# Performance work log

Hardware: AMD Instinct MI355X
Metric: run time of the kernel (lower is better)

The kernel has to match this reference:

```python
import jax, jax.numpy as jnp
import numpy as np

DIM = 192
WIN = 8
HEADS = 6
HEAD_DIM = DIM // HEADS
SCALE = HEAD_DIM ** -0.5
N = WIN * WIN


def _relative_position_index():
    coords = np.stack(np.meshgrid(np.arange(WIN), np.arange(WIN), indexing='ij'))  # [2,W,W]
    flat = coords.reshape(2, -1)  # [2,N]
    rel = flat[:, :, None] - flat[:, None, :]  # [2,N,N]
    rel = rel.transpose(1, 2, 0)
    rel[:, :, 0] += WIN - 1
    rel[:, :, 1] += WIN - 1
    rel[:, :, 0] *= 2 * WIN - 1
    return rel.sum(-1).astype(np.int32)  # [N,N]


def setup_inputs() -> dict:
    key = jax.random.key(0)
    ks = jax.random.split(key, 6)
    B = 4096
    x = jax.random.normal(ks[0], (B, N, DIM), dtype=jnp.float32)
    qkv_w = jax.random.normal(ks[1], (3 * DIM, DIM), dtype=jnp.float32) * (DIM ** -0.5)
    qkv_b = jnp.zeros((3 * DIM,), dtype=jnp.float32)
    proj_w = jax.random.normal(ks[2], (DIM, DIM), dtype=jnp.float32) * (DIM ** -0.5)
    proj_b = jnp.zeros((DIM,), dtype=jnp.float32)
    num_rel = (2 * WIN - 1) * (2 * WIN - 1)
    bias_table = jax.random.normal(ks[3], (num_rel, HEADS), dtype=jnp.float32) * 0.02
    rel_idx = jnp.asarray(_relative_position_index())
    return {"x": x, "qkv_w": qkv_w, "qkv_b": qkv_b, "proj_w": proj_w,
            "proj_b": proj_b, "bias_table": bias_table, "rel_idx": rel_idx}


def reference(x, qkv_w, qkv_b, proj_w, proj_b, bias_table, rel_idx):
    B, n, C = x.shape
    qkv = x @ qkv_w.T + qkv_b  # [B,N,3C]
    qkv = qkv.reshape(B, n, 3, HEADS, HEAD_DIM).transpose(2, 0, 3, 1, 4)  # [3,B,H,N,hd]
    q, k, v = qkv[0], qkv[1], qkv[2]
    attn = jnp.einsum('bhnd,bhmd->bhnm', q * SCALE, k)  # [B,H,N,N]
    bias = bias_table[rel_idx]  # [N,N,H]
    attn = attn + bias.transpose(2, 0, 1)[None]  # add [1,H,N,N]
    attn = jax.nn.softmax(attn, axis=-1)
    out = jnp.einsum('bhnm,bhmd->bhnd', attn, v)
    out = out.transpose(0, 2, 1, 3).reshape(B, n, C)
    return out @ proj_w.T + proj_b
```

## Files before the change

### kernel.cpp

```cpp
#include <hip/hip_runtime.h>

#define NTOK 64
#define DIM 192
#define HEADS 6
#define HD 32
#define SCALE 0.17677669529663687f

typedef __bf16 bf16x8 __attribute__((ext_vector_type(8)));
typedef float f32x4 __attribute__((ext_vector_type(4)));

__device__ __forceinline__ unsigned short f2bf(float f) {
  union { float f; unsigned u; } v; v.f = f;
  unsigned u = v.u;
  return (unsigned short)((u + 0x7FFFu + ((u >> 16) & 1u)) >> 16);
}

__global__ void prep_kernel(const float* __restrict__ qkv_w,
                            const float* __restrict__ proj_w,
                            const float* __restrict__ bias_table,
                            const int* __restrict__ rel_idx,
                            unsigned short* __restrict__ wq,
                            unsigned short* __restrict__ wp,
                            float* __restrict__ biasf) {
  int i = blockIdx.x * 256 + threadIdx.x;
  if (i < 3 * DIM * DIM) wq[i] = f2bf(qkv_w[i]);
  if (i < DIM * DIM) wp[i] = f2bf(proj_w[i]);
  if (i < HEADS * NTOK * NTOK) {
    int h = i >> 12;
    int nm = i & 4095;
    biasf[i] = bias_table[rel_idx[nm] * HEADS + h];
  }
}

__global__ __launch_bounds__(384) void attn_kernel(
    const float* __restrict__ x,
    const float* __restrict__ qkv_b,
    const float* __restrict__ proj_b,
    const unsigned short* __restrict__ wq,
    const unsigned short* __restrict__ wp,
    const float* __restrict__ biasf,
    float* __restrict__ out) {
  __shared__ unsigned short xs[NTOK * 200];
  __shared__ unsigned short qs[HEADS * NTOK * HD];
  __shared__ unsigned short kk[HEADS * NTOK * HD];
  __shared__ unsigned short vts[HEADS * HD * 72];
  __shared__ unsigned short Ps[HEADS * NTOK * 72];

  const int tid = threadIdx.x;
  const int w = tid >> 6;
  const int lane = tid & 63;
  const int l15 = lane & 15;
  const int quad = lane >> 4;
  const long b = blockIdx.x;

  {
    const float4* xg = (const float4*)(x + b * (NTOK * DIM));
    #pragma unroll
    for (int it = 0; it < 8; ++it) {
      int idx = tid + it * 384;
      float4 v = xg[idx];
      int row = idx / 48;
      int col = (idx % 48) * 4;
      ushort4 o;
      o.x = f2bf(v.x); o.y = f2bf(v.y); o.z = f2bf(v.z); o.w = f2bf(v.w);
      *(ushort4*)&xs[row * 200 + col] = o;
    }
  }
  __syncthreads();

  for (int i = 0; i < 6; ++i) {
    int jt = w * 6 + i;
    int j = jt * 16 + l15;
    f32x4 acc[4] = {f32x4{0.f,0.f,0.f,0.f}, f32x4{0.f,0.f,0.f,0.f},
                    f32x4{0.f,0.f,0.f,0.f}, f32x4{0.f,0.f,0.f,0.f}};
    #pragma unroll
    for (int ks = 0; ks < 6; ++ks) {
      bf16x8 bw = *(const bf16x8*)(wq + (size_t)j * DIM + ks * 32 + quad * 8);
      #pragma unroll
      for (int rt = 0; rt < 4; ++rt) {
        bf16x8 a = *(const bf16x8*)&xs[(rt * 16 + l15) * 200 + ks * 32 + quad * 8];
        acc[rt] = __builtin_amdgcn_mfma_f32_16x16x32_bf16(a, bw, acc[rt], 0, 0, 0);
      }
    }
    float bj = qkv_b[j];
    int which = jt / 12;
    int ft = jt % 12;
    int h = ft >> 1;
    int d = (ft & 1) * 16 + l15;
    if (which == 0) {
      #pragma unroll
      for (int rt = 0; rt < 4; ++rt)
        #pragma unroll
        for (int g = 0; g < 4; ++g) {
          int row = rt * 16 + quad * 4 + g;
          qs[(h * NTOK + row) * HD + d] = f2bf((acc[rt][g] + bj) * SCALE);
        }
    } else if (which == 1) {
      #pragma unroll
      for (int rt = 0; rt < 4; ++rt)
        #pragma unroll
        for (int g = 0; g < 4; ++g) {
          int row = rt * 16 + quad * 4 + g;
          kk[(h * NTOK + row) * HD + d] = f2bf(acc[rt][g] + bj);
        }
    } else {
      #pragma unroll
      for (int rt = 0; rt < 4; ++rt) {
        ushort4 o;
        o.x = f2bf(acc[rt][0] + bj);
        o.y = f2bf(acc[rt][1] + bj);
        o.z = f2bf(acc[rt][2] + bj);
        o.w = f2bf(acc[rt][3] + bj);
        int row0 = rt * 16 + quad * 4;
        *(ushort4*)&vts[(h * HD + d) * 72 + row0] = o;
      }
    }
  }
  __syncthreads();

  {
    const int h = w;
    bf16x8 qa[4], kb[4];
    #pragma unroll
    for (int rt = 0; rt < 4; ++rt)
      qa[rt] = *(const bf16x8*)&qs[(h * NTOK + rt * 16 + l15) * HD + quad * 8];
    #pragma unroll
    for (int ct = 0; ct < 4; ++ct)
      kb[ct] = *(const bf16x8*)&kk[(h * NTOK + ct * 16 + l15) * HD + quad * 8];
    f32x4 s[4][4];
    #pragma unroll
    for (int rt = 0; rt < 4; ++rt)
      #pragma unroll
      for (int ct = 0; ct < 4; ++ct) {
        s[rt][ct] = f32x4{0.f, 0.f, 0.f, 0.f};
        s[rt][ct] = __builtin_amdgcn_mfma_f32_16x16x32_bf16(qa[rt], kb[ct], s[rt][ct], 0, 0, 0);
      }
    const float* bh = biasf + h * 4096;
    #pragma unroll
    for (int rt = 0; rt < 4; ++rt) {
      #pragma unroll
      for (int g = 0; g < 4; ++g) {
        int row = rt * 16 + quad * 4 + g;
        const float* bp = bh + row * 64 + l15;
        float v0 = s[rt][0][g] + bp[0];
        float v1 = s[rt][1][g] + bp[16];
        float v2 = s[rt][2][g] + bp[32];
        float v3 = s[rt][3][g] + bp[48];
        float mx = fmaxf(fmaxf(v0, v1), fmaxf(v2, v3));
        mx = fmaxf(mx, __shfl_xor(mx, 1));
        mx = fmaxf(mx, __shfl_xor(mx, 2));
        mx = fmaxf(mx, __shfl_xor(mx, 4));
        mx = fmaxf(mx, __shfl_xor(mx, 8));
        float e0 = __expf(v0 - mx);
        float e1 = __expf(v1 - mx);
        float e2 = __expf(v2 - mx);
        float e3 = __expf(v3 - mx);
        float sm = e0 + e1 + e2 + e3;
        sm += __shfl_xor(sm, 1);
        sm += __shfl_xor(sm, 2);
        sm += __shfl_xor(sm, 4);
        sm += __shfl_xor(sm, 8);
        float r = __builtin_amdgcn_rcpf(sm);
        int base = (h * NTOK + row) * 72 + l15;
        Ps[base + 0]  = f2bf(e0 * r);
        Ps[base + 16] = f2bf(e1 * r);
        Ps[base + 32] = f2bf(e2 * r);
        Ps[base + 48] = f2bf(e3 * r);
      }
    }
    bf16x8 vb[2][2];
    #pragma unroll
    for (int c2 = 0; c2 < 2; ++c2)
      #pragma unroll
      for (int kv = 0; kv < 2; ++kv)
        vb[c2][kv] = *(const bf16x8*)&vts[(h * HD + c2 * 16 + l15) * 72 + kv * 32 + quad * 8];
    f32x4 o[4][2];
    #pragma unroll
    for (int rt = 0; rt < 4; ++rt)
      #pragma unroll
      for (int c2 = 0; c2 < 2; ++c2)
        o[rt][c2] = f32x4{0.f, 0.f, 0.f, 0.f};
    #pragma unroll
    for (int rt = 0; rt < 4; ++rt)
      #pragma unroll
      for (int kv = 0; kv < 2; ++kv) {
        bf16x8 pa = *(const bf16x8*)&Ps[(h * NTOK + rt * 16 + l15) * 72 + kv * 32 + quad * 8];
        #pragma unroll
        for (int c2 = 0; c2 < 2; ++c2)
          o[rt][c2] = __builtin_amdgcn_mfma_f32_16x16x32_bf16(pa, vb[c2][kv], o[rt][c2], 0, 0, 0);
      }
    #pragma unroll
    for (int rt = 0; rt < 4; ++rt)
      #pragma unroll
      for (int c2 = 0; c2 < 2; ++c2)
        #pragma unroll
        for (int g = 0; g < 4; ++g) {
          int row = rt * 16 + quad * 4 + g;
          xs[row * 200 + h * HD + c2 * 16 + l15] = f2bf(o[rt][c2][g]);
        }
  }
  __syncthreads();

  for (int i = 0; i < 2; ++i) {
    int et = w * 2 + i;
    int e = et * 16 + l15;
    f32x4 acc[4] = {f32x4{0.f,0.f,0.f,0.f}, f32x4{0.f,0.f,0.f,0.f},
                    f32x4{0.f,0.f,0.f,0.f}, f32x4{0.f,0.f,0.f,0.f}};
    #pragma unroll
    for (int ks = 0; ks < 6; ++ks) {
      bf16x8 bw = *(const bf16x8*)(wp + (size_t)e * DIM + ks * 32 + quad * 8);
      #pragma unroll
      for (int rt = 0; rt < 4; ++rt) {
        bf16x8 a = *(const bf16x8*)&xs[(rt * 16 + l15) * 200 + ks * 32 + quad * 8];
        acc[rt] = __builtin_amdgcn_mfma_f32_16x16x32_bf16(a, bw, acc[rt], 0, 0, 0);
      }
    }
    float pb = proj_b[e];
    float* og = out + b * (NTOK * DIM);
    #pragma unroll
    for (int rt = 0; rt < 4; ++rt)
      #pragma unroll
      for (int g = 0; g < 4; ++g) {
        int row = rt * 16 + quad * 4 + g;
        og[row * DIM + e] = acc[rt][g] + pb;
      }
  }
}

extern "C" void kernel_launch(void* const* d_in, const int* in_sizes, int n_in,
                              void* d_out, int out_size, void* d_ws, size_t ws_size,
                              hipStream_t stream) {
  const float* x          = (const float*)d_in[0];
  const float* qkv_w      = (const float*)d_in[1];
  const float* qkv_b      = (const float*)d_in[2];
  const float* proj_w     = (const float*)d_in[3];
  const float* proj_b     = (const float*)d_in[4];
  const float* bias_table = (const float*)d_in[5];
  const int*   rel_idx    = (const int*)d_in[6];

  unsigned short* wq = (unsigned short*)d_ws;
  unsigned short* wp = wq + 3 * DIM * DIM;
  float* biasf = (float*)(wp + DIM * DIM);

  prep_kernel<<<432, 256, 0, stream>>>(qkv_w, proj_w, bias_table, rel_idx, wq, wp, biasf);
  attn_kernel<<<4096, 384, 0, stream>>>(x, qkv_b, proj_b, wq, wp, biasf, (float*)d_out);
}
```

Before: 556.9 us.

## Keep per-head Q/K/V and softmax probabilities in registers, dropping LDS staging

Each wave now computes its own head's Q, K and V projections directly into MFMA operand fragments. A permuted row mapping and transposed products (S^T = K·Q^T) line the outputs up as inputs for the next MFMA, so the qs/kk/vts/Ps shared-memory buffers and their intermediate barrier are gone. This cuts LDS footprint (allowing more blocks per CU) and removes LDS round-trips, and the softmax reduction becomes mostly in-lane. The cost is more register pressure, per-wave weight reloads from global/L2 for the head's 96 rows, and an extra barrier before reusing xs for the attention output.

```diff
diff --git a/kernel.cpp b/kernel.cpp
--- a/kernel.cpp
+++ b/kernel.cpp
@@ -5,9 +5,13 @@
 #define HEADS 6
 #define HD 32
 #define SCALE 0.17677669529663687f
+#define XSS 200
 
 typedef __bf16 bf16x8 __attribute__((ext_vector_type(8)));
 typedef float f32x4 __attribute__((ext_vector_type(4)));
+
+union U8 { bf16x8 v; unsigned short s[8]; };
+union F4 { float4 v; float f[4]; };
 
 __device__ __forceinline__ unsigned short f2bf(float f) {
   union { float f; unsigned u; } v; v.f = f;
@@ -40,11 +44,7 @@
     const unsigned short* __restrict__ wp,
     const float* __restrict__ biasf,
     float* __restrict__ out) {
-  __shared__ unsigned short xs[NTOK * 200];
-  __shared__ unsigned short qs[HEADS * NTOK * HD];
-  __shared__ unsigned short kk[HEADS * NTOK * HD];
-  __shared__ unsigned short vts[HEADS * HD * 72];
-  __shared__ unsigned short Ps[HEADS * NTOK * 72];
+  __shared__ unsigned short xs[NTOK * XSS];
 
   const int tid = threadIdx.x;
   const int w = tid >> 6;
@@ -52,6 +52,7 @@
   const int l15 = lane & 15;
   const int quad = lane >> 4;
   const long b = blockIdx.x;
+  const int h = w;
 
   {
     const float4* xg = (const float4*)(x + b * (NTOK * DIM));
@@ -63,167 +64,173 @@
       int col = (idx % 48) * 4;
       ushort4 o;
       o.x = f2bf(v.x); o.y = f2bf(v.y); o.z = f2bf(v.z); o.w = f2bf(v.w);
-      *(ushort4*)&xs[row * 200 + col] = o;
+      *(ushort4*)&xs[row * XSS + col] = o;
     }
   }
   __syncthreads();
 
-  for (int i = 0; i < 6; ++i) {
-    int jt = w * 6 + i;
-    int j = jt * 16 + l15;
-    f32x4 acc[4] = {f32x4{0.f,0.f,0.f,0.f}, f32x4{0.f,0.f,0.f,0.f},
-                    f32x4{0.f,0.f,0.f,0.f}, f32x4{0.f,0.f,0.f,0.f}};
-    #pragma unroll
-    for (int ks = 0; ks < 6; ++ks) {
-      bf16x8 bw = *(const bf16x8*)(wq + (size_t)j * DIM + ks * 32 + quad * 8);
-      #pragma unroll
-      for (int rt = 0; rt < 4; ++rt) {
-        bf16x8 a = *(const bf16x8*)&xs[(rt * 16 + l15) * 200 + ks * 32 + quad * 8];
-        acc[rt] = __builtin_amdgcn_mfma_f32_16x16x32_bf16(a, bw, acc[rt], 0, 0, 0);
-      }
-    }
-    float bj = qkv_b[j];
-    int which = jt / 12;
-    int ft = jt % 12;
-    int h = ft >> 1;
-    int d = (ft & 1) * 16 + l15;
-    if (which == 0) {
-      #pragma unroll
-      for (int rt = 0; rt < 4; ++rt)
+  const int prm = ((l15 >> 2) << 3) | (l15 & 3);
+  const f32x4 zero = {0.f, 0.f, 0.f, 0.f};
+
+  bf16x8 qfrag[4];
+  {
+    const unsigned short* wqh = wq + ((size_t)h * 32) * DIM;
+    F4 qb0, qb1;
+    qb0.v = *(const float4*)(qkv_b + h * 32 + quad * 8);
+    qb1.v = *(const float4*)(qkv_b + h * 32 + quad * 8 + 4);
+    #pragma unroll
+    for (int nt = 0; nt < 4; ++nt) {
+      bf16x8 xn[6];
+      #pragma unroll
+      for (int ks = 0; ks < 6; ++ks)
+        xn[ks] = *(const bf16x8*)&xs[(nt * 16 + l15) * XSS + ks * 32 + quad * 8];
+      f32x4 a0 = zero, a1 = zero;
+      #pragma unroll
+      for (int ks = 0; ks < 6; ++ks) {
+        bf16x8 w0 = *(const bf16x8*)(wqh + (size_t)(prm + 0) * DIM + ks * 32 + quad * 8);
+        bf16x8 w1 = *(const bf16x8*)(wqh + (size_t)(prm + 4) * DIM + ks * 32 + quad * 8);
+        a0 = __builtin_amdgcn_mfma_f32_16x16x32_bf16(w0, xn[ks], a0, 0, 0, 0);
+        a1 = __builtin_amdgcn_mfma_f32_16x16x32_bf16(w1, xn[ks], a1, 0, 0, 0);
+      }
+      U8 t;
+      #pragma unroll
+      for (int g = 0; g < 4; ++g) {
+        t.s[g]     = f2bf((a0[g] + qb0.f[g]) * SCALE);
+        t.s[4 + g] = f2bf((a1[g] + qb1.f[g]) * SCALE);
+      }
+      qfrag[nt] = t.v;
+    }
+  }
+
+  bf16x8 kfrag[4];
+  U8 vbu[2][2];
+  {
+    const unsigned short* wkh = wq + ((size_t)(192 + h * 32)) * DIM;
+    const unsigned short* wvh = wq + ((size_t)(384 + h * 32)) * DIM;
+    F4 kb0, kb1;
+    kb0.v = *(const float4*)(qkv_b + 192 + h * 32 + quad * 8);
+    kb1.v = *(const float4*)(qkv_b + 192 + h * 32 + quad * 8 + 4);
+    const float vbias0 = qkv_b[384 + h * 32 + l15];
+    const float vbias1 = qkv_b[384 + h * 32 + 16 + l15];
+    #pragma unroll
+    for (int mt = 0; mt < 4; ++mt) {
+      const int kv = mt >> 1, half = mt & 1;
+      const int xrow = kv * 32 + half * 4 + prm;
+      bf16x8 xp[6];
+      #pragma unroll
+      for (int ks = 0; ks < 6; ++ks)
+        xp[ks] = *(const bf16x8*)&xs[xrow * XSS + ks * 32 + quad * 8];
+      f32x4 ka0 = zero, ka1 = zero, va0 = zero, va1 = zero;
+      #pragma unroll
+      for (int ks = 0; ks < 6; ++ks) {
+        bf16x8 wk0 = *(const bf16x8*)(wkh + (size_t)(prm + 0) * DIM + ks * 32 + quad * 8);
+        bf16x8 wk1 = *(const bf16x8*)(wkh + (size_t)(prm + 4) * DIM + ks * 32 + quad * 8);
+        bf16x8 wv0 = *(const bf16x8*)(wvh + (size_t)(l15 + 0) * DIM + ks * 32 + quad * 8);
+        bf16x8 wv1 = *(const bf16x8*)(wvh + (size_t)(l15 + 16) * DIM + ks * 32 + quad * 8);
+        ka0 = __builtin_amdgcn_mfma_f32_16x16x32_bf16(wk0, xp[ks], ka0, 0, 0, 0);
+        ka1 = __builtin_amdgcn_mfma_f32_16x16x32_bf16(wk1, xp[ks], ka1, 0, 0, 0);
+        va0 = __builtin_amdgcn_mfma_f32_16x16x32_bf16(xp[ks], wv0, va0, 0, 0, 0);
+        va1 = __builtin_amdgcn_mfma_f32_16x16x32_bf16(xp[ks], wv1, va1, 0, 0, 0);
+      }
+      U8 t;
+      #pragma unroll
+      for (int g = 0; g < 4; ++g) {
+        t.s[g]     = f2bf(ka0[g] + kb0.f[g]);
+        t.s[4 + g] = f2bf(ka1[g] + kb1.f[g]);
+        vbu[0][kv].s[half * 4 + g] = f2bf(va0[g] + vbias0);
+        vbu[1][kv].s[half * 4 + g] = f2bf(va1[g] + vbias1);
+      }
+      kfrag[mt] = t.v;
+    }
+  }
+
+  f32x4 s[4][4];
+  #pragma unroll
+  for (int mt = 0; mt < 4; ++mt)
+    #pragma unroll
+    for (int nt = 0; nt < 4; ++nt)
+      s[mt][nt] = __builtin_amdgcn_mfma_f32_16x16x32_bf16(kfrag[mt], qfrag[nt], zero, 0, 0, 0);
+
+  bf16x8 pa[4][2];
+  {
+    const float* bh = biasf + h * 4096;
+    #pragma unroll
+    for (int nt = 0; nt < 4; ++nt) {
+      float ve[16];
+      #pragma unroll
+      for (int mt = 0; mt < 4; ++mt) {
+        F4 bb;
+        bb.v = *(const float4*)(bh + (nt * 16 + l15) * 64 + (mt >> 1) * 32 + quad * 8 + (mt & 1) * 4);
         #pragma unroll
-        for (int g = 0; g < 4; ++g) {
-          int row = rt * 16 + quad * 4 + g;
-          qs[(h * NTOK + row) * HD + d] = f2bf((acc[rt][g] + bj) * SCALE);
-        }
-    } else if (which == 1) {
-      #pragma unroll
-      for (int rt = 0; rt < 4; ++rt)
+        for (int g = 0; g < 4; ++g) ve[mt * 4 + g] = s[mt][nt][g] + bb.f[g];
+      }
+      float mx = ve[0];
+      #pragma unroll
+      for (int t = 1; t < 16; ++t) mx = fmaxf(mx, ve[t]);
+      mx = fmaxf(mx, __shfl_xor(mx, 16));
+      mx = fmaxf(mx, __shfl_xor(mx, 32));
+      float sm = 0.f;
+      #pragma unroll
+      for (int t = 0; t < 16; ++t) { ve[t] = __expf(ve[t] - mx); sm += ve[t]; }
+      sm += __shfl_xor(sm, 16);
+      sm += __shfl_xor(sm, 32);
+      float r = __builtin_amdgcn_rcpf(sm);
+      U8 t0, t1;
+      #pragma unroll
+      for (int j = 0; j < 8; ++j) {
+        t0.s[j] = f2bf(ve[j] * r);
+        t1.s[j] = f2bf(ve[8 + j] * r);
+      }
+      pa[nt][0] = t0.v;
+      pa[nt][1] = t1.v;
+    }
+  }
+
+  f32x4 o[4][2];
+  #pragma unroll
+  for (int nt = 0; nt < 4; ++nt)
+    #pragma unroll
+    for (int c2 = 0; c2 < 2; ++c2) {
+      f32x4 acc = __builtin_amdgcn_mfma_f32_16x16x32_bf16(pa[nt][0], vbu[c2][0].v, zero, 0, 0, 0);
+      o[nt][c2] = __builtin_amdgcn_mfma_f32_16x16x32_bf16(pa[nt][1], vbu[c2][1].v, acc, 0, 0, 0);
+    }
+
+  __syncthreads();
+  #pragma unroll
+  for (int nt = 0; nt < 4; ++nt)
+    #pragma unroll
+    for (int c2 = 0; c2 < 2; ++c2)
+      #pragma unroll
+      for (int g = 0; g < 4; ++g)
+        xs[(nt * 16 + quad * 4 + g) * XSS + h * 32 + c2 * 16 + l15] = f2bf(o[nt][c2][g]);
+  __syncthreads();
+
+  {
+    bf16x8 af[4][6];
+    #pragma unroll
+    for (int nt = 0; nt < 4; ++nt)
+      #pragma unroll
+      for (int ks = 0; ks < 6; ++ks)
+        af[nt][ks] = *(const bf16x8*)&xs[(nt * 16 + l15) * XSS + ks * 32 + quad * 8];
+    float* og = out + b * (NTOK * DIM);
+    #pragma unroll
+    for (int i = 0; i < 2; ++i) {
+      const int e = w * 32 + i * 16 + l15;
+      f32x4 acc[4] = {zero, zero, zero, zero};
+      #pragma unroll
+      for (int ks = 0; ks < 6; ++ks) {
+        bf16x8 bw = *(const bf16x8*)(wp + (size_t)e * DIM + ks * 32 + quad * 8);
         #pragma unroll
-        for (int g = 0; g < 4; ++g) {
-          int row = rt * 16 + quad * 4 + g;
-          kk[(h * NTOK + row) * HD + d] = f2bf(acc[rt][g] + bj);
-        }
-    } else {
-      #pragma unroll
-      for (int rt = 0; rt < 4; ++rt) {
-        ushort4 o;
-        o.x = f2bf(acc[rt][0] + bj);
-        o.y = f2bf(acc[rt][1] + bj);
-        o.z = f2bf(acc[rt][2] + bj);
-        o.w = f2bf(acc[rt][3] + bj);
-        int row0 = rt * 16 + quad * 4;
-        *(ushort4*)&vts[(h * HD + d) * 72 + row0] = o;
-      }
-    }
-  }
-  __syncthreads();
-
-  {
-    const int h = w;
-    bf16x8 qa[4], kb[4];
-    #pragma unroll
-    for (int rt = 0; rt < 4; ++rt)
-      qa[rt] = *(const bf16x8*)&qs[(h * NTOK + rt * 16 + l15) * HD + quad * 8];
-    #pragma unroll
-    for (int ct = 0; ct < 4; ++ct)
-      kb[ct] = *(const bf16x8*)&kk[(h * NTOK + ct * 16 + l15) * HD + quad * 8];
-    f32x4 s[4][4];
-    #pragma unroll
-    for (int rt = 0; rt < 4; ++rt)
-      #pragma unroll
-      for (int ct = 0; ct < 4; ++ct) {
-        s[rt][ct] = f32x4{0.f, 0.f, 0.f, 0.f};
-        s[rt][ct] = __builtin_amdgcn_mfma_f32_16x16x32_bf16(qa[rt], kb[ct], s[rt][ct], 0, 0, 0);
-      }
-    const float* bh = biasf + h * 4096;
-    #pragma unroll
-    for (int rt = 0; rt < 4; ++rt) {
-      #pragma unroll
-      for (int g = 0; g < 4; ++g) {
-        int row = rt * 16 + quad * 4 + g;
-        const float* bp = bh + row * 64 + l15;
-        float v0 = s[rt][0][g] + bp[0];
-        float v1 = s[rt][1][g] + bp[16];
-        float v2 = s[rt][2][g] + bp[32];
-        float v3 = s[rt][3][g] + bp[48];
-        float mx = fmaxf(fmaxf(v0, v1), fmaxf(v2, v3));
-        mx = fmaxf(mx, __shfl_xor(mx, 1));
-        mx = fmaxf(mx, __shfl_xor(mx, 2));
-        mx = fmaxf(mx, __shfl_xor(mx, 4));
-        mx = fmaxf(mx, __shfl_xor(mx, 8));
-        float e0 = __expf(v0 - mx);
-        float e1 = __expf(v1 - mx);
-        float e2 = __expf(v2 - mx);
-        float e3 = __expf(v3 - mx);
-        float sm = e0 + e1 + e2 + e3;
-        sm += __shfl_xor(sm, 1);
-        sm += __shfl_xor(sm, 2);
-        sm += __shfl_xor(sm, 4);
-        sm += __shfl_xor(sm, 8);
-        float r = __builtin_amdgcn_rcpf(sm);
-        int base = (h * NTOK + row) * 72 + l15;
-        Ps[base + 0]  = f2bf(e0 * r);
-        Ps[base + 16] = f2bf(e1 * r);
-        Ps[base + 32] = f2bf(e2 * r);
-        Ps[base + 48] = f2bf(e3 * r);
-      }
-    }
-    bf16x8 vb[2][2];
-    #pragma unroll
-    for (int c2 = 0; c2 < 2; ++c2)
-      #pragma unroll
-      for (int kv = 0; kv < 2; ++kv)
-        vb[c2][kv] = *(const bf16x8*)&vts[(h * HD + c2 * 16 + l15) * 72 + kv * 32 + quad * 8];
-    f32x4 o[4][2];
-    #pragma unroll
-    for (int rt = 0; rt < 4; ++rt)
-      #pragma unroll
-      for (int c2 = 0; c2 < 2; ++c2)
-        o[rt][c2] = f32x4{0.f, 0.f, 0.f, 0.f};
-    #pragma unroll
-    for (int rt = 0; rt < 4; ++rt)
-      #pragma unroll
-      for (int kv = 0; kv < 2; ++kv) {
-        bf16x8 pa = *(const bf16x8*)&Ps[(h * NTOK + rt * 16 + l15) * 72 + kv * 32 + quad * 8];
+        for (int nt = 0; nt < 4; ++nt)
+          acc[nt] = __builtin_amdgcn_mfma_f32_16x16x32_bf16(af[nt][ks], bw, acc[nt], 0, 0, 0);
+      }
+      const float pb = proj_b[e];
+      #pragma unroll
+      for (int nt = 0; nt < 4; ++nt)
         #pragma unroll
-        for (int c2 = 0; c2 < 2; ++c2)
-          o[rt][c2] = __builtin_amdgcn_mfma_f32_16x16x32_bf16(pa, vb[c2][kv], o[rt][c2], 0, 0, 0);
-      }
-    #pragma unroll
-    for (int rt = 0; rt < 4; ++rt)
-      #pragma unroll
-      for (int c2 = 0; c2 < 2; ++c2)
-        #pragma unroll
-        for (int g = 0; g < 4; ++g) {
-          int row = rt * 16 + quad * 4 + g;
-          xs[row * 200 + h * HD + c2 * 16 + l15] = f2bf(o[rt][c2][g]);
-        }
-  }
-  __syncthreads();
-
-  for (int i = 0; i < 2; ++i) {
-    int et = w * 2 + i;
-    int e = et * 16 + l15;
-    f32x4 acc[4] = {f32x4{0.f,0.f,0.f,0.f}, f32x4{0.f,0.f,0.f,0.f},
-                    f32x4{0.f,0.f,0.f,0.f}, f32x4{0.f,0.f,0.f,0.f}};
-    #pragma unroll
-    for (int ks = 0; ks < 6; ++ks) {
-      bf16x8 bw = *(const bf16x8*)(wp + (size_t)e * DIM + ks * 32 + quad * 8);
-      #pragma unroll
-      for (int rt = 0; rt < 4; ++rt) {
-        bf16x8 a = *(const bf16x8*)&xs[(rt * 16 + l15) * 200 + ks * 32 + quad * 8];
-        acc[rt] = __builtin_amdgcn_mfma_f32_16x16x32_bf16(a, bw, acc[rt], 0, 0, 0);
-      }
-    }
-    float pb = proj_b[e];
-    float* og = out + b * (NTOK * DIM);
-    #pragma unroll
-    for (int rt = 0; rt < 4; ++rt)
-      #pragma unroll
-      for (int g = 0; g < 4; ++g) {
-        int row = rt * 16 + quad * 4 + g;
-        og[row * DIM + e] = acc[rt][g] + pb;
-      }
+        for (int g = 0; g < 4; ++g)
+          og[(nt * 16 + quad * 4 + g) * DIM + e] = acc[nt][g] + pb;
+    }
   }
 }
 
```

After: 523.0 us. 1.06x faster.
